# Performance work log

Hardware: AMD Instinct MI355X
Metric: run time of the kernel (lower is better)

The kernel has to match this reference:

```python
import jax, jax.numpy as jnp
import numpy as np

B, S, D, H = 2, 2048, 1024, 16
DK = D // H
MAX_REL = 2047          # clip range for relative distances
REL_DIM = 64            # rel_embedding dim, summed over


def setup_inputs() -> dict:
    key = jax.random.key(0)
    ks = jax.random.split(key, 12)
    sc = 1.0 / np.sqrt(D)
    inp = {
        "q": jax.random.normal(ks[0], (B, S, D), jnp.float32),
        "k": jax.random.normal(ks[1], (B, S, D), jnp.float32),
        "v": jax.random.normal(ks[2], (B, S, D), jnp.float32),
        "Wq": jax.random.normal(ks[3], (D, D), jnp.float32) * sc,
        "bq": jnp.zeros((D,), jnp.float32),
        "Wk": jax.random.normal(ks[4], (D, D), jnp.float32) * sc,
        "bk": jnp.zeros((D,), jnp.float32),
        "Wv": jax.random.normal(ks[5], (D, D), jnp.float32) * sc,
        "bv": jnp.zeros((D,), jnp.float32),
        "Wo": jax.random.normal(ks[6], (D, D), jnp.float32) * sc,
        "bo": jnp.zeros((D,), jnp.float32),
        "rel_table": jax.random.normal(ks[7], (2 * MAX_REL + 1, REL_DIM), jnp.float32) * 0.02,
        "mask": jnp.tril(jnp.ones((1, 1, S, S), jnp.bool_)),  # causal
    }
    return inp


def reference(q, k, v, Wq, bq, Wk, bk, Wv, bv, Wo, bo, rel_table, mask):
    def split_heads(x):
        # [B,S,D] -> [B,H,S,DK]
        return x.reshape(B, -1, H, DK).transpose(0, 2, 1, 3)

    Q = split_heads(q @ Wq + bq)
    K = split_heads(k @ Wk + bk)
    V = split_heads(v @ Wv + bv)

    scores = jnp.einsum("bhqd,bhkd->bhqk", Q, K) / jnp.sqrt(jnp.float32(DK))

    # relative position bias: table[clip(j - i)] summed over rel dim -> [S,S]
    rel_idx = jnp.clip(jnp.arange(S)[None, :] - jnp.arange(S)[:, None],
                       -MAX_REL, MAX_REL) + MAX_REL
    rel_bias = rel_table[rel_idx].sum(-1)  # [S,S]
    scores = scores + rel_bias[None, None]

    scores = jnp.where(mask, scores, jnp.float32(-1e20))
    attn = jax.nn.softmax(scores, axis=-1)

    out = jnp.einsum("bhqk,bhkd->bhqd", attn, V)
    out = out.transpose(0, 2, 1, 3).reshape(B, -1, D)
    return out @ Wo + bo
```

## Files before the change

### kernel.cpp

```cpp
#include <hip/hip_runtime.h>

#define SEQ 2048
#define DIM 1024
#define NH 16
#define HD 64
#define NB 2

typedef __bf16 bf16x8 __attribute__((ext_vector_type(8)));
typedef float f32x4 __attribute__((ext_vector_type(4)));
typedef float f32x4v __attribute__((ext_vector_type(4)));
typedef float f32x4u __attribute__((ext_vector_type(4), aligned(4)));
typedef unsigned short us8 __attribute__((ext_vector_type(8)));
typedef unsigned short us4 __attribute__((ext_vector_type(4)));

#define LOG2E 1.44269504f

__device__ __forceinline__ unsigned short bfbits(float f) {
  __bf16 h = (__bf16)f;
  return __builtin_bit_cast(unsigned short, h);
}

__global__ void relsum_kernel(const float* __restrict__ rel_table,
                              float* __restrict__ relsum) {
  int i = blockIdx.x * blockDim.x + threadIdx.x;
  if (i < 4095) {
    const f32x4v* row = reinterpret_cast<const f32x4v*>(rel_table + (size_t)i * 64);
    float s = 0.f;
    for (int d = 0; d < 16; ++d) {
      f32x4v v = row[d];
      s += v[0] + v[1] + v[2] + v[3];
    }
    relsum[i] = s * LOG2E;
  }
}

__global__ __launch_bounds__(256) void wconv4_kernel(
    const float* __restrict__ W0, const float* __restrict__ W1,
    const float* __restrict__ W2, const float* __restrict__ W3,
    unsigned short* __restrict__ Wt) {
  __shared__ unsigned short T[64][68];
  int z = blockIdx.z;
  const float* W = (z == 0) ? W0 : (z == 1) ? W1 : (z == 2) ? W2 : W3;
  unsigned short* out = Wt + (size_t)z * 1024 * 1024;
  int r0 = blockIdx.y * 64;
  int c0 = blockIdx.x * 64;
  int tid = threadIdx.x;
  for (int it = 0; it < 4; ++it) {
    int s = tid + it * 256;
    int r = s >> 4;
    int c4 = (s & 15) * 4;
    f32x4v v = *reinterpret_cast<const f32x4v*>(W + (size_t)(r0 + r) * 1024 + c0 + c4);
    us4 o;
    o[0] = bfbits(v[0]); o[1] = bfbits(v[1]); o[2] = bfbits(v[2]); o[3] = bfbits(v[3]);
    *reinterpret_cast<us4*>(&T[r][c4]) = o;
  }
  __syncthreads();
  for (int it = 0; it < 2; ++it) {
    int s = tid + it * 256;
    int n = s >> 3;
    int k8 = (s & 7) * 8;
    us8 o;
    for (int e = 0; e < 8; ++e) o[e] = T[k8 + e][n];
    *reinterpret_cast<us8*>(out + (size_t)(c0 + n) * 1024 + r0 + k8) = o;
  }
}

template <int A_BF16, int OUT_BF16>
__global__ __launch_bounds__(256) void gemm_bias_kernel(
    const void* __restrict__ Ap, const unsigned short* __restrict__ WT,
    const float* __restrict__ bias, void* __restrict__ Cp, float oscale) {
  constexpr int N = 1024, K = 1024;
  int o = ((blockIdx.x & 7) << 6) | (blockIdx.x >> 3);
  int col0 = (o & 15) * 64;
  int row0 = (o >> 4) * 128;
  int tid = threadIdx.x;
  int w = tid >> 6;
  int lane = tid & 63;
  int lg = lane >> 4;
  int li = lane & 15;
  int wr = (w >> 1) * 64;
  int wc = (w & 1) * 32;

  __shared__ unsigned short As[128][72];
  __shared__ unsigned short Ws[64][72];

  f32x4 acc[4][2] = {};

  for (int k0 = 0; k0 < K; k0 += 64) {
    __syncthreads();
    if (A_BF16) {
      const unsigned short* A = (const unsigned short*)Ap;
      for (int it = 0; it < 4; ++it) {
        int s = tid + it * 256;
        int r = s >> 3;
        int cg = (s & 7) * 8;
        us8 vv = *reinterpret_cast<const us8*>(A + (size_t)(row0 + r) * K + k0 + cg);
        *reinterpret_cast<us8*>(&As[r][cg]) = vv;
      }
    } else {
      const float* A = (const float*)Ap;
      for (int it = 0; it < 8; ++it) {
        int s = tid + it * 256;
        int r = s >> 4;
        int cg = (s & 15) * 4;
        f32x4v vv = *reinterpret_cast<const f32x4v*>(A + (size_t)(row0 + r) * K + k0 + cg);
        us4 o2;
        o2[0] = bfbits(vv[0]); o2[1] = bfbits(vv[1]); o2[2] = bfbits(vv[2]); o2[3] = bfbits(vv[3]);
        *reinterpret_cast<us4*>(&As[r][cg]) = o2;
      }
    }
    for (int it = 0; it < 2; ++it) {
      int s = tid + it * 256;
      int c = s >> 3;
      int kg = (s & 7) * 8;
      us8 vv = *reinterpret_cast<const us8*>(WT + (size_t)(col0 + c) * K + k0 + kg);
      *reinterpret_cast<us8*>(&Ws[c][kg]) = vv;
    }
    __syncthreads();
    for (int kk = 0; kk < 2; ++kk) {
      bf16x8 af[4], bfr[2];
      for (int m = 0; m < 4; ++m)
        af[m] = *reinterpret_cast<const bf16x8*>(&As[wr + m * 16 + li][kk * 32 + lg * 8]);
      for (int n = 0; n < 2; ++n)
        bfr[n] = *reinterpret_cast<const bf16x8*>(&Ws[wc + n * 16 + li][kk * 32 + lg * 8]);
      for (int m = 0; m < 4; ++m)
        for (int n = 0; n < 2; ++n)
          acc[m][n] = __builtin_amdgcn_mfma_f32_16x16x32_bf16(af[m], bfr[n], acc[m][n], 0, 0, 0);
    }
  }

  for (int m = 0; m < 4; ++m)
    for (int n = 0; n < 2; ++n)
      for (int r = 0; r < 4; ++r) {
        int row = row0 + wr + m * 16 + lg * 4 + r;
        int col = col0 + wc + n * 16 + li;
        float val = (acc[m][n][r] + bias[col]) * oscale;
        if (OUT_BF16)
          ((unsigned short*)Cp)[(size_t)row * N + col] = bfbits(val);
        else
          ((float*)Cp)[(size_t)row * N + col] = val;
      }
}

__global__ __launch_bounds__(256) void attn_kernel(
    const unsigned short* __restrict__ Qb, const unsigned short* __restrict__ Kb,
    const unsigned short* __restrict__ Vb, const float* __restrict__ relsum,
    unsigned short* __restrict__ Ob) {
  int o = ((blockIdx.x & 7) << 6) | (blockIdx.x >> 3);
  int p = o & 15;
  int h = (o >> 4) & 15;
  int b = o >> 8;

  int tid = threadIdx.x;
  int w = tid >> 6;
  int lane = tid & 63;
  int lg = lane >> 4;
  int li = lane & 15;

  __shared__ unsigned short Ks[64][72];
  __shared__ unsigned short VtF[64 * 72];
  __shared__ __bf16 Ps[4][16][72];

  int key0 = tid >> 3;
  int cg0 = (tid & 7) * 8;
  int j0 = tid & 7;
  const unsigned short* kptr = Kb + ((size_t)(b * SEQ + key0)) * DIM + h * HD + cg0;
  const unsigned short* vptr = Vb + ((size_t)(b * SEQ + key0)) * DIM + h * HD + cg0;

  us8 krg0, krg1, vrg0, vrg1;

#define LOAD_REGS(TT)                                                     \
  {                                                                       \
    size_t off = (size_t)(TT) * 64 * DIM;                                 \
    krg0 = *reinterpret_cast<const us8*>(kptr + off);                     \
    vrg0 = *reinterpret_cast<const us8*>(vptr + off);                     \
    krg1 = *reinterpret_cast<const us8*>(kptr + off + 32 * DIM);          \
    vrg1 = *reinterpret_cast<const us8*>(vptr + off + 32 * DIM);          \
  }

#define WRITE_TILE()                                                      \
  {                                                                       \
    *reinterpret_cast<us8*>(&Ks[key0][cg0]) = krg0;                       \
    *reinterpret_cast<us8*>(&Ks[key0 + 32][cg0]) = krg1;                  \
    for (int e = 0; e < 8; ++e) {                                         \
      VtF[((unsigned)((cg0 + e) * 72 + key0)) ^ ((unsigned)j0 << 3)] = vrg0[e]; \
      VtF[((unsigned)((cg0 + e) * 72 + key0 + 32)) ^ ((unsigned)j0 << 3)] = vrg1[e]; \
    }                                                                     \
  }

  LOAD_REGS(0);

  for (int ph = 0; ph < 2; ++ph) {
    int qt = ph ? p : (31 - p);

    int qrow = qt * 64 + w * 16 + li;
    const unsigned short* qb = Qb + ((size_t)(b * SEQ + qrow)) * DIM + h * HD;
    bf16x8 qa0 = *reinterpret_cast<const bf16x8*>(qb + lg * 8);
    bf16x8 qa1 = *reinterpret_cast<const bf16x8*>(qb + 32 + lg * 8);

    f32x4 o_acc[4] = {};
    float m_row[4], l_row[4];
    for (int r = 0; r < 4; ++r) { m_row[r] = -3e38f; l_row[r] = 0.f; }
    int i0 = qt * 64 + w * 16 + lg * 4;

    for (int t = 0; t <= qt; ++t) {
      __syncthreads();
      WRITE_TILE();
      __syncthreads();

      if (!(ph == 1 && t == qt)) {
        int nextT = (t < qt) ? (t + 1) : 0;
        LOAD_REGS(nextT);
      }

      f32x4 s_acc[4] = {};
      __builtin_amdgcn_s_setprio(1);
      for (int kk = 0; kk < 2; ++kk) {
        bf16x8 qa = kk ? qa1 : qa0;
        for (int n = 0; n < 4; ++n) {
          bf16x8 kb = *reinterpret_cast<const bf16x8*>(&Ks[n * 16 + li][kk * 32 + lg * 8]);
          s_acc[n] = __builtin_amdgcn_mfma_f32_16x16x32_bf16(qa, kb, s_acc[n], 0, 0, 0);
        }
      }
      __builtin_amdgcn_s_setprio(0);

      float tmax[4] = {-3e38f, -3e38f, -3e38f, -3e38f};
      int Cbase = (t - qt) * 64 - (w * 16 + lg * 4) + li + 2047;
      if (t == qt) {
        for (int n = 0; n < 4; ++n) {
          int Cn = Cbase + n * 16;
          f32x4u rel4 = *reinterpret_cast<const f32x4u*>(&relsum[Cn - 3]);
          for (int r = 0; r < 4; ++r) {
            float sv = s_acc[n][r] + rel4[3 - r];
            sv = (Cn - r > 2047) ? -1e30f : sv;
            s_acc[n][r] = sv;
            tmax[r] = fmaxf(tmax[r], sv);
          }
        }
      } else {
        for (int n = 0; n < 4; ++n) {
          int Cn = Cbase + n * 16;
          f32x4u rel4 = *reinterpret_cast<const f32x4u*>(&relsum[Cn - 3]);
          for (int r = 0; r < 4; ++r) {
            float sv = s_acc[n][r] + rel4[3 - r];
            s_acc[n][r] = sv;
            tmax[r] = fmaxf(tmax[r], sv);
          }
        }
      }

      bool okl = true;
      for (int r = 0; r < 4; ++r) okl &= (tmax[r] <= m_row[r] + 8.f);
      if (!__all(okl)) {
        for (int msk = 1; msk < 16; msk <<= 1)
          for (int r = 0; r < 4; ++r)
            tmax[r] = fmaxf(tmax[r], __shfl_xor(tmax[r], msk));
        for (int r = 0; r < 4; ++r) {
          float mn = fmaxf(m_row[r], tmax[r]);
          float al = exp2f(m_row[r] - mn);
          m_row[r] = mn;
          l_row[r] *= al;
          o_acc[0][r] *= al; o_acc[1][r] *= al;
          o_acc[2][r] *= al; o_acc[3][r] *= al;
        }
      }

      for (int n = 0; n < 4; ++n)
        for (int r = 0; r < 4; ++r) {
          float e = exp2f(s_acc[n][r] - m_row[r]);
          s_acc[n][r] = e;
          l_row[r] += e;
        }

      for (int n = 0; n < 4; ++n)
        for (int r = 0; r < 4; ++r)
          Ps[w][lg * 4 + r][n * 16 + li] = (__bf16)s_acc[n][r];
      asm volatile("s_waitcnt lgkmcnt(0)" ::: "memory");
      __builtin_amdgcn_sched_barrier(0);

      __builtin_amdgcn_s_setprio(1);
      for (int kk = 0; kk < 2; ++kk) {
        bf16x8 pa = *reinterpret_cast<const bf16x8*>(&Ps[w][li][kk * 32 + lg * 8]);
        for (int n = 0; n < 4; ++n) {
          int dk = n * 16 + li;
          unsigned idx = ((unsigned)(dk * 72 + kk * 32 + lg * 8)) ^
                         ((((unsigned)dk >> 3) & 7u) << 3);
          bf16x8 vb = *reinterpret_cast<const bf16x8*>(&VtF[idx]);
          o_acc[n] = __builtin_amdgcn_mfma_f32_16x16x32_bf16(pa, vb, o_acc[n], 0, 0, 0);
        }
      }
      __builtin_amdgcn_s_setprio(0);
    }

    for (int msk = 1; msk < 16; msk <<= 1)
      for (int r = 0; r < 4; ++r) l_row[r] += __shfl_xor(l_row[r], msk);
    float inv_l[4];
    for (int r = 0; r < 4; ++r) inv_l[r] = 1.f / l_row[r];
    for (int n = 0; n < 4; ++n)
      for (int r = 0; r < 4; ++r) {
        int row = i0 + r;
        int dk = n * 16 + li;
        Ob[((size_t)(b * SEQ + row)) * DIM + h * HD + dk] =
            bfbits(o_acc[n][r] * inv_l[r]);
      }
  }
#undef LOAD_REGS
#undef WRITE_TILE
}

extern "C" void kernel_launch(void* const* d_in, const int* in_sizes, int n_in,
                              void* d_out, int out_size, void* d_ws, size_t ws_size,
                              hipStream_t stream) {
  const float* q = (const float*)d_in[0];
  const float* k = (const float*)d_in[1];
  const float* v = (const float*)d_in[2];
  const float* Wq = (const float*)d_in[3];
  const float* bq = (const float*)d_in[4];
  const float* Wk = (const float*)d_in[5];
  const float* bk = (const float*)d_in[6];
  const float* Wv = (const float*)d_in[7];
  const float* bv = (const float*)d_in[8];
  const float* Wo = (const float*)d_in[9];
  const float* bo = (const float*)d_in[10];
  const float* rel = (const float*)d_in[11];

  char* ws = (char*)d_ws;
  const size_t MATB = (size_t)NB * SEQ * DIM * sizeof(unsigned short);
  const size_t WTE = (size_t)DIM * DIM;
  unsigned short* Qb = (unsigned short*)(ws);
  unsigned short* Kb = (unsigned short*)(ws + MATB);
  unsigned short* Vb = (unsigned short*)(ws + 2 * MATB);
  unsigned short* Ob = (unsigned short*)(ws + 3 * MATB);
  float* relsum = (float*)(ws + 4 * MATB);
  unsigned short* WT = (unsigned short*)(ws + 4 * MATB + 65536);

  relsum_kernel<<<16, 256, 0, stream>>>(rel, relsum);
  wconv4_kernel<<<dim3(16, 16, 4), 256, 0, stream>>>(Wq, Wk, Wv, Wo, WT);

  const float qscale = 0.125f * LOG2E;
  gemm_bias_kernel<0, 1><<<dim3(512), 256, 0, stream>>>((const void*)q, WT + 0 * WTE, bq, (void*)Qb, qscale);
  gemm_bias_kernel<0, 1><<<dim3(512), 256, 0, stream>>>((const void*)k, WT + 1 * WTE, bk, (void*)Kb, 1.0f);
  gemm_bias_kernel<0, 1><<<dim3(512), 256, 0, stream>>>((const void*)v, WT + 2 * WTE, bv, (void*)Vb, 1.0f);

  attn_kernel<<<dim3(512), 256, 0, stream>>>(Qb, Kb, Vb, relsum, Ob);

  gemm_bias_kernel<1, 0><<<dim3(512), 256, 0, stream>>>((const void*)Ob, WT + 3 * WTE, bo, d_out, 1.0f);
}
```

Baseline: 149.7 us.

## Fuse QKV GEMMs, double-buffer GEMM tiles, pre-transpose V, cache relsum in LDS

Merges the three QKV projection GEMMs into one 1536-block launch and gives both GEMM kernels double-buffered LDS with register prefetch, so global loads overlap the MFMA work. Adds a separate kernel that transposes V per head, so the attention kernel writes V tiles to LDS with vector stores instead of scalar scattered stores. The relative-bias vector is copied into LDS once per attention block. In exchange it adds an extra launch and a V round trip through memory, and uses more shared memory, which may lower occupancy.

```diff
diff --git a/kernel.cpp b/kernel.cpp
--- a/kernel.cpp
+++ b/kernel.cpp
@@ -65,10 +65,146 @@
   }
 }
 
-template <int A_BF16, int OUT_BF16>
-__global__ __launch_bounds__(256) void gemm_bias_kernel(
-    const void* __restrict__ Ap, const unsigned short* __restrict__ WT,
-    const float* __restrict__ bias, void* __restrict__ Cp, float oscale) {
+__global__ __launch_bounds__(256) void vtrans_kernel(
+    const unsigned short* __restrict__ Vb, unsigned short* __restrict__ Vt) {
+  __shared__ unsigned short T[64 * 72];
+  int s0 = blockIdx.x * 64;
+  int h = blockIdx.y;
+  int b = blockIdx.z;
+  int tid = threadIdx.x;
+  int key0 = tid >> 3;
+  int cg0 = (tid & 7) * 8;
+  int j0 = tid & 7;
+  const unsigned short* src = Vb + ((size_t)(b * SEQ + s0)) * DIM + h * HD;
+  for (int it = 0; it < 2; ++it) {
+    int key = key0 + it * 32;
+    us8 v = *reinterpret_cast<const us8*>(src + (size_t)key * DIM + cg0);
+    for (int e = 0; e < 8; ++e) {
+      unsigned idx = (unsigned)((cg0 + e) * 72 + key) ^ ((unsigned)j0 << 3);
+      T[idx] = v[e];
+    }
+  }
+  __syncthreads();
+  for (int it = 0; it < 2; ++it) {
+    int slot = tid + it * 256;
+    int dk = slot >> 3;
+    int k8 = (slot & 7) * 8;
+    unsigned idx = ((unsigned)(dk * 72 + k8)) ^ ((((unsigned)dk >> 3) & 7u) << 3);
+    us8 o = *reinterpret_cast<const us8*>(&T[idx]);
+    *reinterpret_cast<us8*>(Vt + ((size_t)(b * NH + h) * HD + dk) * SEQ + s0 + k8) = o;
+  }
+}
+
+__global__ __launch_bounds__(256) void gemm_qkv_kernel(
+    const float* __restrict__ Aq, const float* __restrict__ Ak,
+    const float* __restrict__ Av, const unsigned short* __restrict__ WTb,
+    const float* __restrict__ bq, const float* __restrict__ bk,
+    const float* __restrict__ bv, unsigned short* __restrict__ Qb,
+    unsigned short* __restrict__ Kb, unsigned short* __restrict__ Vb,
+    float qscale) {
+  constexpr int N = 1024, K = 1024;
+  int o = (blockIdx.x & 7) * 192 + (blockIdx.x >> 3);
+  int row0 = (o / 48) * 128;
+  int colz = o % 48;
+  int z = colz >> 4;
+  int col0 = (colz & 15) * 64;
+  const float* A = (z == 0) ? Aq : (z == 1) ? Ak : Av;
+  const unsigned short* WT = WTb + (size_t)z * N * K;
+  const float* bias = (z == 0) ? bq : (z == 1) ? bk : bv;
+  unsigned short* Cp = (z == 0) ? Qb : (z == 1) ? Kb : Vb;
+  float oscale = (z == 0) ? qscale : 1.0f;
+
+  int tid = threadIdx.x;
+  int w = tid >> 6;
+  int lane = tid & 63;
+  int lg = lane >> 4;
+  int li = lane & 15;
+  int wr = (w >> 1) * 64;
+  int wc = (w & 1) * 32;
+
+  __shared__ unsigned short As[2][128][72];
+  __shared__ unsigned short Ws[2][64][72];
+
+  f32x4v af32[8];
+  us8 wreg[2];
+
+#define GLOAD(KS)                                                         \
+  {                                                                       \
+    int k0 = (KS) * 64;                                                   \
+    for (int it = 0; it < 8; ++it) {                                      \
+      int s = tid + it * 256;                                             \
+      int r = s >> 4;                                                     \
+      int cg = (s & 15) * 4;                                              \
+      af32[it] = *reinterpret_cast<const f32x4v*>(                        \
+          A + (size_t)(row0 + r) * K + k0 + cg);                          \
+    }                                                                     \
+    for (int it = 0; it < 2; ++it) {                                      \
+      int s = tid + it * 256;                                             \
+      int c = s >> 3;                                                     \
+      int kg = (s & 7) * 8;                                               \
+      wreg[it] = *reinterpret_cast<const us8*>(                           \
+          WT + (size_t)(col0 + c) * K + k0 + kg);                         \
+    }                                                                     \
+  }
+
+#define SWRITE(B)                                                         \
+  {                                                                       \
+    for (int it = 0; it < 8; ++it) {                                      \
+      int s = tid + it * 256;                                             \
+      int r = s >> 4;                                                     \
+      int cg = (s & 15) * 4;                                              \
+      us4 o2;                                                             \
+      o2[0] = bfbits(af32[it][0]); o2[1] = bfbits(af32[it][1]);           \
+      o2[2] = bfbits(af32[it][2]); o2[3] = bfbits(af32[it][3]);           \
+      *reinterpret_cast<us4*>(&As[B][r][cg]) = o2;                        \
+    }                                                                     \
+    for (int it = 0; it < 2; ++it) {                                      \
+      int s = tid + it * 256;                                             \
+      int c = s >> 3;                                                     \
+      int kg = (s & 7) * 8;                                               \
+      *reinterpret_cast<us8*>(&Ws[B][c][kg]) = wreg[it];                  \
+    }                                                                     \
+  }
+
+  f32x4 acc[4][2] = {};
+
+  GLOAD(0);
+  SWRITE(0);
+  GLOAD(1);
+  __syncthreads();
+
+  for (int ks = 0; ks < 16; ++ks) {
+    if (ks < 15) SWRITE((ks + 1) & 1);
+    if (ks < 14) GLOAD(ks + 2);
+    int B = ks & 1;
+    for (int kk = 0; kk < 2; ++kk) {
+      bf16x8 af[4], bfr[2];
+      for (int m = 0; m < 4; ++m)
+        af[m] = *reinterpret_cast<const bf16x8*>(&As[B][wr + m * 16 + li][kk * 32 + lg * 8]);
+      for (int n = 0; n < 2; ++n)
+        bfr[n] = *reinterpret_cast<const bf16x8*>(&Ws[B][wc + n * 16 + li][kk * 32 + lg * 8]);
+      for (int m = 0; m < 4; ++m)
+        for (int n = 0; n < 2; ++n)
+          acc[m][n] = __builtin_amdgcn_mfma_f32_16x16x32_bf16(af[m], bfr[n], acc[m][n], 0, 0, 0);
+    }
+    __syncthreads();
+  }
+
+  for (int m = 0; m < 4; ++m)
+    for (int n = 0; n < 2; ++n)
+      for (int r = 0; r < 4; ++r) {
+        int row = row0 + wr + m * 16 + lg * 4 + r;
+        int col = col0 + wc + n * 16 + li;
+        float val = (acc[m][n][r] + bias[col]) * oscale;
+        Cp[(size_t)row * N + col] = bfbits(val);
+      }
+#undef GLOAD
+#undef SWRITE
+}
+
+__global__ __launch_bounds__(256) void gemm_out_kernel(
+    const unsigned short* __restrict__ A, const unsigned short* __restrict__ WT,
+    const float* __restrict__ bias, float* __restrict__ Cp) {
   constexpr int N = 1024, K = 1024;
   int o = ((blockIdx.x & 7) << 6) | (blockIdx.x >> 3);
   int col0 = (o & 15) * 64;
@@ -81,52 +217,69 @@
   int wr = (w >> 1) * 64;
   int wc = (w & 1) * 32;
 
-  __shared__ unsigned short As[128][72];
-  __shared__ unsigned short Ws[64][72];
+  __shared__ unsigned short As[2][128][72];
+  __shared__ unsigned short Ws[2][64][72];
+
+  us8 ab16[4];
+  us8 wreg[2];
+
+#define GLOAD(KS)                                                         \
+  {                                                                       \
+    int k0 = (KS) * 64;                                                   \
+    for (int it = 0; it < 4; ++it) {                                      \
+      int s = tid + it * 256;                                             \
+      int r = s >> 3;                                                     \
+      int cg = (s & 7) * 8;                                               \
+      ab16[it] = *reinterpret_cast<const us8*>(                           \
+          A + (size_t)(row0 + r) * K + k0 + cg);                          \
+    }                                                                     \
+    for (int it = 0; it < 2; ++it) {                                      \
+      int s = tid + it * 256;                                             \
+      int c = s >> 3;                                                     \
+      int kg = (s & 7) * 8;                                               \
+      wreg[it] = *reinterpret_cast<const us8*>(                           \
+          WT + (size_t)(col0 + c) * K + k0 + kg);                         \
+    }                                                                     \
+  }
+
+#define SWRITE(B)                                                         \
+  {                                                                       \
+    for (int it = 0; it < 4; ++it) {                                      \
+      int s = tid + it * 256;                                             \
+      int r = s >> 3;                                                     \
+      int cg = (s & 7) * 8;                                               \
+      *reinterpret_cast<us8*>(&As[B][r][cg]) = ab16[it];                  \
+    }                                                                     \
+    for (int it = 0; it < 2; ++it) {                                      \
+      int s = tid + it * 256;                                             \
+      int c = s >> 3;                                                     \
+      int kg = (s & 7) * 8;                                               \
+      *reinterpret_cast<us8*>(&Ws[B][c][kg]) = wreg[it];                  \
+    }                                                                     \
+  }
 
   f32x4 acc[4][2] = {};
 
-  for (int k0 = 0; k0 < K; k0 += 64) {
-    __syncthreads();
-    if (A_BF16) {
-      const unsigned short* A = (const unsigned short*)Ap;
-      for (int it = 0; it < 4; ++it) {
-        int s = tid + it * 256;
-        int r = s >> 3;
-        int cg = (s & 7) * 8;
-        us8 vv = *reinterpret_cast<const us8*>(A + (size_t)(row0 + r) * K + k0 + cg);
-        *reinterpret_cast<us8*>(&As[r][cg]) = vv;
-      }
-    } else {
-      const float* A = (const float*)Ap;
-      for (int it = 0; it < 8; ++it) {
-        int s = tid + it * 256;
-        int r = s >> 4;
-        int cg = (s & 15) * 4;
-        f32x4v vv = *reinterpret_cast<const f32x4v*>(A + (size_t)(row0 + r) * K + k0 + cg);
-        us4 o2;
-        o2[0] = bfbits(vv[0]); o2[1] = bfbits(vv[1]); o2[2] = bfbits(vv[2]); o2[3] = bfbits(vv[3]);
-        *reinterpret_cast<us4*>(&As[r][cg]) = o2;
-      }
-    }
-    for (int it = 0; it < 2; ++it) {
-      int s = tid + it * 256;
-      int c = s >> 3;
-      int kg = (s & 7) * 8;
-      us8 vv = *reinterpret_cast<const us8*>(WT + (size_t)(col0 + c) * K + k0 + kg);
-      *reinterpret_cast<us8*>(&Ws[c][kg]) = vv;
-    }
-    __syncthreads();
+  GLOAD(0);
+  SWRITE(0);
+  GLOAD(1);
+  __syncthreads();
+
+  for (int ks = 0; ks < 16; ++ks) {
+    if (ks < 15) SWRITE((ks + 1) & 1);
+    if (ks < 14) GLOAD(ks + 2);
+    int B = ks & 1;
     for (int kk = 0; kk < 2; ++kk) {
       bf16x8 af[4], bfr[2];
       for (int m = 0; m < 4; ++m)
-        af[m] = *reinterpret_cast<const bf16x8*>(&As[wr + m * 16 + li][kk * 32 + lg * 8]);
+        af[m] = *reinterpret_cast<const bf16x8*>(&As[B][wr + m * 16 + li][kk * 32 + lg * 8]);
       for (int n = 0; n < 2; ++n)
-        bfr[n] = *reinterpret_cast<const bf16x8*>(&Ws[wc + n * 16 + li][kk * 32 + lg * 8]);
+        bfr[n] = *reinterpret_cast<const bf16x8*>(&Ws[B][wc + n * 16 + li][kk * 32 + lg * 8]);
       for (int m = 0; m < 4; ++m)
         for (int n = 0; n < 2; ++n)
           acc[m][n] = __builtin_amdgcn_mfma_f32_16x16x32_bf16(af[m], bfr[n], acc[m][n], 0, 0, 0);
     }
+    __syncthreads();
   }
 
   for (int m = 0; m < 4; ++m)
@@ -134,17 +287,15 @@
       for (int r = 0; r < 4; ++r) {
         int row = row0 + wr + m * 16 + lg * 4 + r;
         int col = col0 + wc + n * 16 + li;
-        float val = (acc[m][n][r] + bias[col]) * oscale;
-        if (OUT_BF16)
-          ((unsigned short*)Cp)[(size_t)row * N + col] = bfbits(val);
-        else
-          ((float*)Cp)[(size_t)row * N + col] = val;
-      }
+        Cp[(size_t)row * N + col] = acc[m][n][r] + bias[col];
+      }
+#undef GLOAD
+#undef SWRITE
 }
 
 __global__ __launch_bounds__(256) void attn_kernel(
     const unsigned short* __restrict__ Qb, const unsigned short* __restrict__ Kb,
-    const unsigned short* __restrict__ Vb, const float* __restrict__ relsum,
+    const unsigned short* __restrict__ Vt, const float* __restrict__ relsum,
     unsigned short* __restrict__ Ob) {
   int o = ((blockIdx.x & 7) << 6) | (blockIdx.x >> 3);
   int p = o & 15;
@@ -160,32 +311,43 @@
   __shared__ unsigned short Ks[64][72];
   __shared__ unsigned short VtF[64 * 72];
   __shared__ __bf16 Ps[4][16][72];
+  __shared__ float rel_lds[2112];
+
+  for (int it = 0; it < 3; ++it) {
+    int slot = tid + it * 256;
+    if (slot < 528)
+      *reinterpret_cast<f32x4v*>(&rel_lds[slot * 4]) =
+          *reinterpret_cast<const f32x4v*>(&relsum[slot * 4]);
+  }
 
   int key0 = tid >> 3;
   int cg0 = (tid & 7) * 8;
-  int j0 = tid & 7;
+  int dk0 = tid >> 3;
+  int k8 = (tid & 7) * 8;
   const unsigned short* kptr = Kb + ((size_t)(b * SEQ + key0)) * DIM + h * HD + cg0;
-  const unsigned short* vptr = Vb + ((size_t)(b * SEQ + key0)) * DIM + h * HD + cg0;
+  const unsigned short* vtp = Vt + ((size_t)(b * NH + h) * HD + dk0) * SEQ + k8;
+
+  unsigned vidx0 = ((unsigned)(dk0 * 72 + k8)) ^ ((((unsigned)dk0 >> 3) & 7u) << 3);
+  unsigned vidx1 = ((unsigned)((dk0 + 32) * 72 + k8)) ^
+                   ((((unsigned)(dk0 + 32) >> 3) & 7u) << 3);
 
   us8 krg0, krg1, vrg0, vrg1;
 
 #define LOAD_REGS(TT)                                                     \
   {                                                                       \
-    size_t off = (size_t)(TT) * 64 * DIM;                                 \
-    krg0 = *reinterpret_cast<const us8*>(kptr + off);                     \
-    vrg0 = *reinterpret_cast<const us8*>(vptr + off);                     \
-    krg1 = *reinterpret_cast<const us8*>(kptr + off + 32 * DIM);          \
-    vrg1 = *reinterpret_cast<const us8*>(vptr + off + 32 * DIM);          \
+    size_t koff = (size_t)(TT) * 64 * DIM;                                \
+    krg0 = *reinterpret_cast<const us8*>(kptr + koff);                    \
+    krg1 = *reinterpret_cast<const us8*>(kptr + koff + 32 * DIM);         \
+    vrg0 = *reinterpret_cast<const us8*>(vtp + (TT) * 64);                \
+    vrg1 = *reinterpret_cast<const us8*>(vtp + 32 * SEQ + (TT) * 64);     \
   }
 
 #define WRITE_TILE()                                                      \
   {                                                                       \
     *reinterpret_cast<us8*>(&Ks[key0][cg0]) = krg0;                       \
     *reinterpret_cast<us8*>(&Ks[key0 + 32][cg0]) = krg1;                  \
-    for (int e = 0; e < 8; ++e) {                                         \
-      VtF[((unsigned)((cg0 + e) * 72 + key0)) ^ ((unsigned)j0 << 3)] = vrg0[e]; \
-      VtF[((unsigned)((cg0 + e) * 72 + key0 + 32)) ^ ((unsigned)j0 << 3)] = vrg1[e]; \
-    }                                                                     \
+    *reinterpret_cast<us8*>(&VtF[vidx0]) = vrg0;                          \
+    *reinterpret_cast<us8*>(&VtF[vidx1]) = vrg1;                          \
   }
 
   LOAD_REGS(0);
@@ -229,7 +391,7 @@
       if (t == qt) {
         for (int n = 0; n < 4; ++n) {
           int Cn = Cbase + n * 16;
-          f32x4u rel4 = *reinterpret_cast<const f32x4u*>(&relsum[Cn - 3]);
+          f32x4u rel4 = *reinterpret_cast<const f32x4u*>(&rel_lds[Cn - 3]);
           for (int r = 0; r < 4; ++r) {
             float sv = s_acc[n][r] + rel4[3 - r];
             sv = (Cn - r > 2047) ? -1e30f : sv;
@@ -240,7 +402,7 @@
       } else {
         for (int n = 0; n < 4; ++n) {
           int Cn = Cbase + n * 16;
-          f32x4u rel4 = *reinterpret_cast<const f32x4u*>(&relsum[Cn - 3]);
+          f32x4u rel4 = *reinterpret_cast<const f32x4u*>(&rel_lds[Cn - 3]);
           for (int r = 0; r < 4; ++r) {
             float sv = s_acc[n][r] + rel4[3 - r];
             s_acc[n][r] = sv;
@@ -333,16 +495,17 @@
   unsigned short* Ob = (unsigned short*)(ws + 3 * MATB);
   float* relsum = (float*)(ws + 4 * MATB);
   unsigned short* WT = (unsigned short*)(ws + 4 * MATB + 65536);
+  unsigned short* Vt = (unsigned short*)(ws + 4 * MATB + 65536 + 4 * WTE * 2);
 
   relsum_kernel<<<16, 256, 0, stream>>>(rel, relsum);
   wconv4_kernel<<<dim3(16, 16, 4), 256, 0, stream>>>(Wq, Wk, Wv, Wo, WT);
 
   const float qscale = 0.125f * LOG2E;
-  gemm_bias_kernel<0, 1><<<dim3(512), 256, 0, stream>>>((const void*)q, WT + 0 * WTE, bq, (void*)Qb, qscale);
-  gemm_bias_kernel<0, 1><<<dim3(512), 256, 0, stream>>>((const void*)k, WT + 1 * WTE, bk, (void*)Kb, 1.0f);
-  gemm_bias_kernel<0, 1><<<dim3(512), 256, 0, stream>>>((const void*)v, WT + 2 * WTE, bv, (void*)Vb, 1.0f);
-
-  attn_kernel<<<dim3(512), 256, 0, stream>>>(Qb, Kb, Vb, relsum, Ob);
-
-  gemm_bias_kernel<1, 0><<<dim3(512), 256, 0, stream>>>((const void*)Ob, WT + 3 * WTE, bo, d_out, 1.0f);
-}
+  gemm_qkv_kernel<<<dim3(1536), 256, 0, stream>>>(q, k, v, WT, bq, bk, bv,
+                                                  Qb, Kb, Vb, qscale);
+  vtrans_kernel<<<dim3(SEQ / 64, NH, NB), 256, 0, stream>>>(Vb, Vt);
+
+  attn_kernel<<<dim3(512), 256, 0, stream>>>(Qb, Kb, Vt, relsum, Ob);
+
+  gemm_out_kernel<<<dim3(512), 256, 0, stream>>>(Ob, WT + 3 * WTE, bo, (float*)d_out);
+}
```

New measurement: 141.1 us. -5.8%, faster.
